# Kernel tuning notes

Hardware: AMD Instinct MI355X
Metric: run time of the kernel (lower is better)

Reference implementation:

```python
import jax, jax.numpy as jnp
import numpy as np

N_NODES = 100000
N_EDGES = 3200000


def spmm(row, col, val, x):
    # out[i] = sum_{e: row[e]==i} val[e] * x[col[e]]  -- sparse adj @ x
    return jax.ops.segment_sum(val[:, None] * x[col], row, num_segments=N_NODES)


def setup_inputs() -> dict:
    key = jax.random.key(0)
    k1, k2, k3, k4, k5, k6 = jax.random.split(key, 6)
    out_feat, hid_feat, in_feat = 32, 64, 128
    # xavier_uniform bounds
    b1 = float(np.sqrt(6.0 / (out_feat + hid_feat)))
    b2 = float(np.sqrt(6.0 / (hid_feat + in_feat)))
    return {
        "feat": jax.random.normal(k1, (N_NODES, out_feat), dtype=jnp.float32),
        "W1": jax.random.uniform(k2, (out_feat, hid_feat), minval=-b1, maxval=b1, dtype=jnp.float32),
        "W2": jax.random.uniform(k3, (hid_feat, in_feat), minval=-b2, maxval=b2, dtype=jnp.float32),
        "edge_row": jax.random.randint(k4, (N_EDGES,), 0, N_NODES, dtype=jnp.int32),
        "edge_col": jax.random.randint(k5, (N_EDGES,), 0, N_NODES, dtype=jnp.int32),
        "edge_val": jax.random.uniform(k6, (N_EDGES,), dtype=jnp.float32),
    }


def reference(feat, W1, W2, edge_row, edge_col, edge_val):
    x = feat @ W1                                  # [N, hid]
    x = spmm(edge_row, edge_col, edge_val, x)      # adj @ x
    # add_act=False: no activation
    x = x @ W2                                     # [N, in_feat]
    x = spmm(edge_row, edge_col, edge_val, x)      # adj @ x
    return x
```

## Files before the change

### kernel.cpp

```cpp
#include <hip/hip_runtime.h>

#define N_NODES 100000
#define N_EDGES 3200000
#define RPB 128
#define NB ((N_NODES + RPB - 1) / RPB)
#define SC_BLOCKS 288
#define SC_PER ((N_EDGES + SC_BLOCKS - 1) / SC_BLOCKS)
#define RS_CAP 6144

typedef unsigned short ushort_t;
typedef unsigned int uint_t;

__device__ __forceinline__ ushort_t f32_to_bf16_rne(float f) {
    uint_t b = __float_as_uint(f);
    return (ushort_t)((b + 0x7FFFu + ((b >> 16) & 1u)) >> 16);
}
__device__ __forceinline__ float bf16_lo(uint_t u) {
    return __uint_as_float(u << 16);
}
__device__ __forceinline__ float bf16_hi(uint_t u) {
    return __uint_as_float(u & 0xffff0000u);
}


__global__ void gemm_w12_kernel(const float* __restrict__ W1,
                                const float* __restrict__ W2,
                                float* __restrict__ W12) {
    int idx = blockIdx.x * blockDim.x + threadIdx.x;
    if (idx >= 32 * 128) return;
    int r = idx >> 7;
    int c = idx & 127;
    float acc = 0.f;
#pragma unroll
    for (int k = 0; k < 64; ++k) acc += W1[r * 64 + k] * W2[k * 128 + c];
    W12[idx] = acc;
}

__global__ void cvt_bf16_kernel(const float* __restrict__ in, ushort_t* __restrict__ ob) {
    int i = blockIdx.x * blockDim.x + threadIdx.x;
    if (i < N_NODES * 32) ob[i] = f32_to_bf16_rne(in[i]);
}

__global__ void gemm_out_kernel(const float* __restrict__ g2,
                                const float* __restrict__ W12,
                                float* __restrict__ out) {
    int tid = threadIdx.x;
    int jo = (tid & 31) * 4;
    int rl = tid >> 5;
    float4 w[32];
#pragma unroll
    for (int k = 0; k < 32; ++k) w[k] = *(const float4*)&W12[k * 128 + jo];
    for (int r = blockIdx.x * 8 + rl; r < N_NODES; r += gridDim.x * 8) {
        const float4* g4 = (const float4*)(g2 + (size_t)r * 32);
        float4 acc = make_float4(0.f, 0.f, 0.f, 0.f);
#pragma unroll
        for (int q = 0; q < 8; ++q) {
            float4 gv = g4[q];
            int k = q * 4;
            acc.x += gv.x * w[k].x;     acc.y += gv.x * w[k].y;
            acc.z += gv.x * w[k].z;     acc.w += gv.x * w[k].w;
            acc.x += gv.y * w[k + 1].x; acc.y += gv.y * w[k + 1].y;
            acc.z += gv.y * w[k + 1].z; acc.w += gv.y * w[k + 1].w;
            acc.x += gv.z * w[k + 2].x; acc.y += gv.z * w[k + 2].y;
            acc.z += gv.z * w[k + 2].z; acc.w += gv.z * w[k + 2].w;
            acc.x += gv.w * w[k + 3].x; acc.y += gv.w * w[k + 3].y;
            acc.z += gv.w * w[k + 3].z; acc.w += gv.w * w[k + 3].w;
        }
        *(float4*)&out[(size_t)r * 128 + jo] = acc;
    }
}


__global__ void hist_bucket_kernel(const int* __restrict__ row, int* __restrict__ cnt) {
    __shared__ int h[NB];
    for (int t = threadIdx.x; t < NB; t += blockDim.x) h[t] = 0;
    __syncthreads();
    int per = (N_EDGES + gridDim.x - 1) / gridDim.x;
    int s = blockIdx.x * per;
    int e = min(s + per, N_EDGES);
    for (int i = s + threadIdx.x; i < e; i += blockDim.x)
        atomicAdd(&h[row[i] >> 7], 1);
    __syncthreads();
    for (int t = threadIdx.x; t < NB; t += blockDim.x)
        if (h[t]) atomicAdd(&cnt[t], h[t]);
}

__global__ void scan_bucket_kernel(const int* __restrict__ cnt,
                                   int* __restrict__ offs, int* __restrict__ cur_b) {
    __shared__ int s[1024];
    int t = threadIdx.x;
    int v = (t < NB) ? cnt[t] : 0;
    s[t] = v;
    __syncthreads();
    for (int off = 1; off < 1024; off <<= 1) {
        int add = (t >= off) ? s[t - off] : 0;
        __syncthreads();
        s[t] += add;
        __syncthreads();
    }
    if (t < NB) { int x = s[t] - v; offs[t] = x; cur_b[t] = x; }
    if (t == 0) offs[NB] = N_EDGES;
}

__global__ void __launch_bounds__(1024, 1)
scatter_stage_kernel(const int* __restrict__ row, const int* __restrict__ col,
                     const float* __restrict__ val,
                     int* __restrict__ cur_b, int2* __restrict__ ebuf) {
    __shared__ int2 payload[SC_PER];
    __shared__ ushort_t bkt[SC_PER];
    __shared__ int h[NB];
    __shared__ int lbase[NB];
    __shared__ int gbase[NB];
    __shared__ int scan_s[1024];
    int t = threadIdx.x;
    int s = blockIdx.x * SC_PER;
    int e = min(s + SC_PER, N_EDGES);
    int n = e - s;
    for (int i = t; i < NB; i += 1024) h[i] = 0;
    __syncthreads();
    for (int i = t; i < n; i += 1024) atomicAdd(&h[row[s + i] >> 7], 1);
    __syncthreads();
    int v = (t < NB) ? h[t] : 0;
    scan_s[t] = v;
    __syncthreads();
    for (int off = 1; off < 1024; off <<= 1) {
        int add = (t >= off) ? scan_s[t - off] : 0;
        __syncthreads();
        scan_s[t] += add;
        __syncthreads();
    }
    if (t < NB) {
        lbase[t] = scan_s[t] - v;
        gbase[t] = v ? atomicAdd(&cur_b[t], v) : 0;
        h[t] = 0;
    }
    __syncthreads();
    for (int i = t; i < n; i += 1024) {
        int r = row[s + i];
        int b = r >> 7;
        int lp = atomicAdd(&h[b], 1);
        int slot = lbase[b] + lp;
        payload[slot] = make_int2((col[s + i] << 7) | (r & 127), __float_as_int(val[s + i]));
        bkt[slot] = (ushort_t)b;
    }
    __syncthreads();
    for (int i = t; i < n; i += 1024) {
        int b = bkt[i];
        ebuf[gbase[b] + (i - lbase[b])] = payload[i];
    }
}

__global__ void rowsort_stage_kernel(const int* __restrict__ offs, const int2* __restrict__ ebuf,
                                     int2* __restrict__ ep, int* __restrict__ rs) {
    __shared__ int h[RPB];
    __shared__ int loff[RPB];
    __shared__ int curl[RPB];
    __shared__ ushort_t perm[RS_CAP];
    int b = blockIdx.x;
    int s = offs[b], e = offs[b + 1];
    int n = e - s;
    int t = threadIdx.x;
    if (t < RPB) h[t] = 0;
    __syncthreads();
    for (int i = t; i < n; i += blockDim.x)
        atomicAdd(&h[ebuf[s + i].x & 127], 1);
    __syncthreads();
    if (t < RPB) loff[t] = h[t];
    __syncthreads();
    for (int off = 1; off < RPB; off <<= 1) {
        int add = (t < RPB && t >= off) ? loff[t - off] : 0;
        __syncthreads();
        if (t < RPB) loff[t] += add;
        __syncthreads();
    }
    if (t < RPB) {
        int excl = loff[t] - h[t];
        curl[t] = excl;
        int r = b * RPB + t;
        if (r < N_NODES) rs[r] = s + excl;
    }
    if (b == 0 && t == 0) rs[N_NODES] = N_EDGES;
    __syncthreads();
    if (n <= RS_CAP) {
        for (int i = t; i < n; i += blockDim.x) {
            int rl = ebuf[s + i].x & 127;
            int lp = atomicAdd(&curl[rl], 1);
            perm[lp] = (ushort_t)i;
        }
        __syncthreads();
        for (int i = t; i < n; i += blockDim.x) {
            int2 cv = ebuf[s + perm[i]];
            ep[s + i] = make_int2(cv.x >> 7, cv.y);
        }
    } else {
        for (int i = t; i < n; i += blockDim.x) {
            int2 cv = ebuf[s + i];
            int rl = cv.x & 127;
            int pos = s + atomicAdd(&curl[rl], 1);
            ep[pos] = make_int2(cv.x >> 7, cv.y);
        }
    }
}

template <bool OUT_BF16>
__global__ void spmm_csr_kernel(const int* __restrict__ rs,
                                const int2* __restrict__ ep,
                                const uint_t* __restrict__ xb,
                                void* __restrict__ outv) {
    int gid = blockIdx.x * blockDim.x + threadIdx.x;
    int wid = gid >> 6;
    int nwaves = (gridDim.x * blockDim.x) >> 6;
    int lane = threadIdx.x & 63;
    int j2 = lane & 15;
    int g = lane >> 4;
    for (int r = wid; r < N_NODES; r += nwaves) {
        int s = rs[r], e = rs[r + 1];
        float a0 = 0.f, a1 = 0.f, b0 = 0.f, b1 = 0.f;
        int p = s + g;
        for (; p + 28 < e; p += 32) {
            int2 c0 = ep[p];
            int2 c1 = ep[p + 4];
            int2 c2 = ep[p + 8];
            int2 c3 = ep[p + 12];
            int2 c4 = ep[p + 16];
            int2 c5 = ep[p + 20];
            int2 c6 = ep[p + 24];
            int2 c7 = ep[p + 28];
            uint_t u0 = xb[c0.x * 16 + j2];
            uint_t u1 = xb[c1.x * 16 + j2];
            uint_t u2 = xb[c2.x * 16 + j2];
            uint_t u3 = xb[c3.x * 16 + j2];
            uint_t u4 = xb[c4.x * 16 + j2];
            uint_t u5 = xb[c5.x * 16 + j2];
            uint_t u6 = xb[c6.x * 16 + j2];
            uint_t u7 = xb[c7.x * 16 + j2];
            float w0 = __int_as_float(c0.y);
            float w1 = __int_as_float(c1.y);
            float w2 = __int_as_float(c2.y);
            float w3 = __int_as_float(c3.y);
            float w4 = __int_as_float(c4.y);
            float w5 = __int_as_float(c5.y);
            float w6 = __int_as_float(c6.y);
            float w7 = __int_as_float(c7.y);
            a0 += w0 * bf16_lo(u0); a1 += w0 * bf16_hi(u0);
            b0 += w1 * bf16_lo(u1); b1 += w1 * bf16_hi(u1);
            a0 += w2 * bf16_lo(u2); a1 += w2 * bf16_hi(u2);
            b0 += w3 * bf16_lo(u3); b1 += w3 * bf16_hi(u3);
            a0 += w4 * bf16_lo(u4); a1 += w4 * bf16_hi(u4);
            b0 += w5 * bf16_lo(u5); b1 += w5 * bf16_hi(u5);
            a0 += w6 * bf16_lo(u6); a1 += w6 * bf16_hi(u6);
            b0 += w7 * bf16_lo(u7); b1 += w7 * bf16_hi(u7);
        }
        for (; p < e; p += 4) {
            int2 cv = ep[p];
            uint_t u = xb[cv.x * 16 + j2];
            float w = __int_as_float(cv.y);
            a0 += w * bf16_lo(u);
            a1 += w * bf16_hi(u);
        }
        float r0 = a0 + b0;
        float r1 = a1 + b1;
        r0 += __shfl_xor(r0, 16, 64);
        r0 += __shfl_xor(r0, 32, 64);
        r1 += __shfl_xor(r1, 16, 64);
        r1 += __shfl_xor(r1, 32, 64);
        if (g == 0) {
            if constexpr (OUT_BF16) {
                uint_t pk = (uint_t)f32_to_bf16_rne(r0) | ((uint_t)f32_to_bf16_rne(r1) << 16);
                ((uint_t*)outv)[r * 16 + j2] = pk;
            } else {
                ((float2*)outv)[r * 16 + j2] = make_float2(r0, r1);
            }
        }
    }
}

__global__ void spmm32_atomic_kernel(const int* __restrict__ row,
                                     const int* __restrict__ col,
                                     const float* __restrict__ val,
                                     const float* __restrict__ x,
                                     float* __restrict__ out) {
    int id = blockIdx.x * blockDim.x + threadIdx.x;
    int e = id >> 5;
    int j = id & 31;
    if (e >= N_EDGES) return;
    atomicAdd(&out[row[e] * 32 + j], val[e] * x[col[e] * 32 + j]);
}

__global__ void gemm_out_fallback_kernel(const float* __restrict__ g2,
                                         const float* __restrict__ W12,
                                         float* __restrict__ out) {
    int id = blockIdx.x * blockDim.x + threadIdx.x;
    int i = id >> 7;
    int j = id & 127;
    const float* g = g2 + i * 32;
    float acc = 0.f;
#pragma unroll
    for (int k = 0; k < 32; ++k) acc += g[k] * W12[k * 128 + j];
    out[id] = acc;
}

extern "C" void kernel_launch(void* const* d_in, const int* in_sizes, int n_in,
                              void* d_out, int out_size, void* d_ws, size_t ws_size,
                              hipStream_t stream) {
    const float* feat = (const float*)d_in[0];
    const float* W1   = (const float*)d_in[1];
    const float* W2   = (const float*)d_in[2];
    const int*   erow = (const int*)d_in[3];
    const int*   ecol = (const int*)d_in[4];
    const float* eval_= (const float*)d_in[5];
    float* out = (float*)d_out;

    float*    W12   = (float*)d_ws;
    ushort_t* xb    = (ushort_t*)(W12 + 4096);
    ushort_t* g1b   = xb + (size_t)N_NODES * 32;
    float*    g2    = (float*)(g1b + (size_t)N_NODES * 32);
    int2*     ep    = (int2*)(g2 + (size_t)N_NODES * 32);
    int*      cnt   = (int*)(ep + N_EDGES);
    int*      offs  = cnt + NB;
    int*      cur_b = offs + NB + 1;
    int*      rs    = cur_b + NB;
    size_t    needed = (size_t)((char*)(rs + N_NODES + 2) - (char*)d_ws);

    int2* ebuf = (int2*)d_out;

    gemm_w12_kernel<<<16, 256, 0, stream>>>(W1, W2, W12);

    if (ws_size >= needed) {
        cvt_bf16_kernel<<<(N_NODES * 32 + 255) / 256, 256, 0, stream>>>(feat, xb);

        hipMemsetAsync(cnt, 0, NB * sizeof(int), stream);
        hist_bucket_kernel<<<256, 1024, 0, stream>>>(erow, cnt);
        scan_bucket_kernel<<<1, 1024, 0, stream>>>(cnt, offs, cur_b);
        scatter_stage_kernel<<<SC_BLOCKS, 1024, 0, stream>>>(erow, ecol, eval_, cur_b, ebuf);
        rowsort_stage_kernel<<<NB, 512, 0, stream>>>(offs, ebuf, ep, rs);

        spmm_csr_kernel<true><<<2048, 256, 0, stream>>>(rs, ep, (const uint_t*)xb, g1b);
        spmm_csr_kernel<false><<<2048, 256, 0, stream>>>(rs, ep, (const uint_t*)g1b, g2);

        gemm_out_kernel<<<1024, 256, 0, stream>>>(g2, W12, out);
    } else {
        float* g1f = (float*)d_ws + 4096;
        float* g2f = g1f + (size_t)N_NODES * 32;
        hipMemsetAsync(g1f, 0, (size_t)N_NODES * 32 * 2 * sizeof(float), stream);
        spmm32_atomic_kernel<<<(N_EDGES * 32) / 256, 256, 0, stream>>>(erow, ecol, eval_, feat, g1f);
        spmm32_atomic_kernel<<<(N_EDGES * 32) / 256, 256, 0, stream>>>(erow, ecol, eval_, g1f, g2f);
        gemm_out_fallback_kernel<<<(N_NODES * 128) / 256, 256, 0, stream>>>(g2f, W12, out);
    }
}
```

Baseline: 262.4 us.

## Fuse prelude kernels, stage rowsort payload in LDS, fuse second SpMM with output GEMM

Merges the W12 product, bf16 conversion and bucket histogram into one launch. The rowsort stage now caches each bucket's edges in shared memory so the permuted copy reads LDS instead of re-reading global memory, with the capacity lowered to fit. The second SpMM now multiplies its 32-wide row result by W12 held in shared memory and writes the 128-wide output directly, which removes the g2 round trip and the separate output GEMM. The trade-off is larger LDS use per block, which may reduce occupancy, plus extra shuffle work per row.

Measured after the change: 286.6 us. +9.3%, slower.

```diff
diff --git a/kernel.cpp b/kernel.cpp
--- a/kernel.cpp
+++ b/kernel.cpp
@@ -6,7 +6,10 @@
 #define NB ((N_NODES + RPB - 1) / RPB)
 #define SC_BLOCKS 288
 #define SC_PER ((N_EDGES + SC_BLOCKS - 1) / SC_BLOCKS)
-#define RS_CAP 6144
+#define RS_CAP 4608
+#define W12_B 16
+#define CVT_B 12500
+#define HIST_B 1024
 
 typedef unsigned short ushort_t;
 typedef unsigned int uint_t;
@@ -22,67 +25,38 @@
     return __uint_as_float(u & 0xffff0000u);
 }
 
-
-__global__ void gemm_w12_kernel(const float* __restrict__ W1,
-                                const float* __restrict__ W2,
-                                float* __restrict__ W12) {
-    int idx = blockIdx.x * blockDim.x + threadIdx.x;
-    if (idx >= 32 * 128) return;
-    int r = idx >> 7;
-    int c = idx & 127;
-    float acc = 0.f;
+__global__ void prelude_kernel(const float* __restrict__ W1, const float* __restrict__ W2,
+                               float* __restrict__ W12,
+                               const float* __restrict__ feat, ushort_t* __restrict__ xb,
+                               const int* __restrict__ row, int* __restrict__ cnt) {
+    int b = blockIdx.x;
+    int t = threadIdx.x;
+    if (b < W12_B) {
+        int idx = b * 256 + t;
+        if (idx < 32 * 128) {
+            int r = idx >> 7;
+            int c = idx & 127;
+            float acc = 0.f;
 #pragma unroll
-    for (int k = 0; k < 64; ++k) acc += W1[r * 64 + k] * W2[k * 128 + c];
-    W12[idx] = acc;
-}
-
-__global__ void cvt_bf16_kernel(const float* __restrict__ in, ushort_t* __restrict__ ob) {
-    int i = blockIdx.x * blockDim.x + threadIdx.x;
-    if (i < N_NODES * 32) ob[i] = f32_to_bf16_rne(in[i]);
-}
-
-__global__ void gemm_out_kernel(const float* __restrict__ g2,
-                                const float* __restrict__ W12,
-                                float* __restrict__ out) {
-    int tid = threadIdx.x;
-    int jo = (tid & 31) * 4;
-    int rl = tid >> 5;
-    float4 w[32];
-#pragma unroll
-    for (int k = 0; k < 32; ++k) w[k] = *(const float4*)&W12[k * 128 + jo];
-    for (int r = blockIdx.x * 8 + rl; r < N_NODES; r += gridDim.x * 8) {
-        const float4* g4 = (const float4*)(g2 + (size_t)r * 32);
-        float4 acc = make_float4(0.f, 0.f, 0.f, 0.f);
-#pragma unroll
-        for (int q = 0; q < 8; ++q) {
-            float4 gv = g4[q];
-            int k = q * 4;
-            acc.x += gv.x * w[k].x;     acc.y += gv.x * w[k].y;
-            acc.z += gv.x * w[k].z;     acc.w += gv.x * w[k].w;
-            acc.x += gv.y * w[k + 1].x; acc.y += gv.y * w[k + 1].y;
-            acc.z += gv.y * w[k + 1].z; acc.w += gv.y * w[k + 1].w;
-            acc.x += gv.z * w[k + 2].x; acc.y += gv.z * w[k + 2].y;
-            acc.z += gv.z * w[k + 2].z; acc.w += gv.z * w[k + 2].w;
-            acc.x += gv.w * w[k + 3].x; acc.y += gv.w * w[k + 3].y;
-            acc.z += gv.w * w[k + 3].z; acc.w += gv.w * w[k + 3].w;
-        }
-        *(float4*)&out[(size_t)r * 128 + jo] = acc;
-    }
-}
-
-
-__global__ void hist_bucket_kernel(const int* __restrict__ row, int* __restrict__ cnt) {
-    __shared__ int h[NB];
-    for (int t = threadIdx.x; t < NB; t += blockDim.x) h[t] = 0;
-    __syncthreads();
-    int per = (N_EDGES + gridDim.x - 1) / gridDim.x;
-    int s = blockIdx.x * per;
-    int e = min(s + per, N_EDGES);
-    for (int i = s + threadIdx.x; i < e; i += blockDim.x)
-        atomicAdd(&h[row[i] >> 7], 1);
-    __syncthreads();
-    for (int t = threadIdx.x; t < NB; t += blockDim.x)
-        if (h[t]) atomicAdd(&cnt[t], h[t]);
+            for (int k = 0; k < 64; ++k) acc += W1[r * 64 + k] * W2[k * 128 + c];
+            W12[idx] = acc;
+        }
+    } else if (b < W12_B + CVT_B) {
+        int i = (b - W12_B) * 256 + t;
+        if (i < N_NODES * 32) xb[i] = f32_to_bf16_rne(feat[i]);
+    } else {
+        __shared__ int h[NB];
+        for (int i = t; i < NB; i += 256) h[i] = 0;
+        __syncthreads();
+        int hb = b - W12_B - CVT_B;
+        int per = N_EDGES / HIST_B;
+        int s = hb * per;
+        int e = min(s + per, N_EDGES);
+        for (int i = s + t; i < e; i += 256) atomicAdd(&h[row[i] >> 7], 1);
+        __syncthreads();
+        for (int i = t; i < NB; i += 256)
+            if (h[i]) atomicAdd(&cnt[i], h[i]);
+    }
 }
 
 __global__ void scan_bucket_kernel(const int* __restrict__ cnt,
@@ -152,18 +126,28 @@
 
 __global__ void rowsort_stage_kernel(const int* __restrict__ offs, const int2* __restrict__ ebuf,
                                      int2* __restrict__ ep, int* __restrict__ rs) {
+    __shared__ int2 pay[RS_CAP];
+    __shared__ ushort_t perm[RS_CAP];
     __shared__ int h[RPB];
     __shared__ int loff[RPB];
     __shared__ int curl[RPB];
-    __shared__ ushort_t perm[RS_CAP];
     int b = blockIdx.x;
     int s = offs[b], e = offs[b + 1];
     int n = e - s;
     int t = threadIdx.x;
     if (t < RPB) h[t] = 0;
     __syncthreads();
-    for (int i = t; i < n; i += blockDim.x)
-        atomicAdd(&h[ebuf[s + i].x & 127], 1);
+    bool fits = (n <= RS_CAP);
+    if (fits) {
+        for (int i = t; i < n; i += blockDim.x) {
+            int2 cv = ebuf[s + i];
+            pay[i] = cv;
+            atomicAdd(&h[cv.x & 127], 1);
+        }
+    } else {
+        for (int i = t; i < n; i += blockDim.x)
+            atomicAdd(&h[ebuf[s + i].x & 127], 1);
+    }
     __syncthreads();
     if (t < RPB) loff[t] = h[t];
     __syncthreads();
@@ -181,15 +165,14 @@
     }
     if (b == 0 && t == 0) rs[N_NODES] = N_EDGES;
     __syncthreads();
-    if (n <= RS_CAP) {
+    if (fits) {
         for (int i = t; i < n; i += blockDim.x) {
-            int rl = ebuf[s + i].x & 127;
-            int lp = atomicAdd(&curl[rl], 1);
+            int lp = atomicAdd(&curl[pay[i].x & 127], 1);
             perm[lp] = (ushort_t)i;
         }
         __syncthreads();
         for (int i = t; i < n; i += blockDim.x) {
-            int2 cv = ebuf[s + perm[i]];
+            int2 cv = pay[perm[i]];
             ep[s + i] = make_int2(cv.x >> 7, cv.y);
         }
     } else {
@@ -202,11 +185,10 @@
     }
 }
 
-template <bool OUT_BF16>
 __global__ void spmm_csr_kernel(const int* __restrict__ rs,
                                 const int2* __restrict__ ep,
                                 const uint_t* __restrict__ xb,
-                                void* __restrict__ outv) {
+                                uint_t* __restrict__ outb) {
     int gid = blockIdx.x * blockDim.x + threadIdx.x;
     int wid = gid >> 6;
     int nwaves = (gridDim.x * blockDim.x) >> 6;
@@ -265,14 +247,103 @@
         r1 += __shfl_xor(r1, 16, 64);
         r1 += __shfl_xor(r1, 32, 64);
         if (g == 0) {
-            if constexpr (OUT_BF16) {
-                uint_t pk = (uint_t)f32_to_bf16_rne(r0) | ((uint_t)f32_to_bf16_rne(r1) << 16);
-                ((uint_t*)outv)[r * 16 + j2] = pk;
-            } else {
-                ((float2*)outv)[r * 16 + j2] = make_float2(r0, r1);
-            }
-        }
-    }
+            uint_t pk = (uint_t)f32_to_bf16_rne(r0) | ((uint_t)f32_to_bf16_rne(r1) << 16);
+            outb[r * 16 + j2] = pk;
+        }
+    }
+}
+
+__global__ void spmm_fused_kernel(const int* __restrict__ rs,
+                                  const int2* __restrict__ ep,
+                                  const uint_t* __restrict__ xb,
+                                  const float* __restrict__ W12,
+                                  float* __restrict__ out) {
+    __shared__ float w12s[32 * 128];
+    for (int i = threadIdx.x; i < 32 * 128; i += blockDim.x) w12s[i] = W12[i];
+    __syncthreads();
+    int gid = blockIdx.x * blockDim.x + threadIdx.x;
+    int wid = gid >> 6;
+    int nwaves = (gridDim.x * blockDim.x) >> 6;
+    int lane = threadIdx.x & 63;
+    int j2 = lane & 15;
+    int g = lane >> 4;
+    int c0 = lane * 2;
+    for (int r = wid; r < N_NODES; r += nwaves) {
+        int s = rs[r], e = rs[r + 1];
+        float a0 = 0.f, a1 = 0.f, b0 = 0.f, b1 = 0.f;
+        int p = s + g;
+        for (; p + 28 < e; p += 32) {
+            int2 e0 = ep[p];
+            int2 e1 = ep[p + 4];
+            int2 e2 = ep[p + 8];
+            int2 e3 = ep[p + 12];
+            int2 e4 = ep[p + 16];
+            int2 e5 = ep[p + 20];
+            int2 e6 = ep[p + 24];
+            int2 e7 = ep[p + 28];
+            uint_t u0 = xb[e0.x * 16 + j2];
+            uint_t u1 = xb[e1.x * 16 + j2];
+            uint_t u2 = xb[e2.x * 16 + j2];
+            uint_t u3 = xb[e3.x * 16 + j2];
+            uint_t u4 = xb[e4.x * 16 + j2];
+            uint_t u5 = xb[e5.x * 16 + j2];
+            uint_t u6 = xb[e6.x * 16 + j2];
+            uint_t u7 = xb[e7.x * 16 + j2];
+            float w0 = __int_as_float(e0.y);
+            float w1 = __int_as_float(e1.y);
+            float w2 = __int_as_float(e2.y);
+            float w3 = __int_as_float(e3.y);
+            float w4 = __int_as_float(e4.y);
+            float w5 = __int_as_float(e5.y);
+            float w6 = __int_as_float(e6.y);
+            float w7 = __int_as_float(e7.y);
+            a0 += w0 * bf16_lo(u0); a1 += w0 * bf16_hi(u0);
+            b0 += w1 * bf16_lo(u1); b1 += w1 * bf16_hi(u1);
+            a0 += w2 * bf16_lo(u2); a1 += w2 * bf16_hi(u2);
+            b0 += w3 * bf16_lo(u3); b1 += w3 * bf16_hi(u3);
+            a0 += w4 * bf16_lo(u4); a1 += w4 * bf16_hi(u4);
+            b0 += w5 * bf16_lo(u5); b1 += w5 * bf16_hi(u5);
+            a0 += w6 * bf16_lo(u6); a1 += w6 * bf16_hi(u6);
+            b0 += w7 * bf16_lo(u7); b1 += w7 * bf16_hi(u7);
+        }
+        for (; p < e; p += 4) {
+            int2 cv = ep[p];
+            uint_t u = xb[cv.x * 16 + j2];
+            float w = __int_as_float(cv.y);
+            a0 += w * bf16_lo(u);
+            a1 += w * bf16_hi(u);
+        }
+        float r0 = a0 + b0;
+        float r1 = a1 + b1;
+        r0 += __shfl_xor(r0, 16, 64);
+        r0 += __shfl_xor(r0, 32, 64);
+        r1 += __shfl_xor(r1, 16, 64);
+        r1 += __shfl_xor(r1, 32, 64);
+        float o0 = 0.f, o1 = 0.f;
+#pragma unroll
+        for (int k = 0; k < 16; ++k) {
+            float ga = __shfl(r0, k, 64);
+            float gb = __shfl(r1, k, 64);
+            float2 wa = *(const float2*)&w12s[(2 * k) * 128 + c0];
+            float2 wb = *(const float2*)&w12s[(2 * k + 1) * 128 + c0];
+            o0 += ga * wa.x + gb * wb.x;
+            o1 += ga * wa.y + gb * wb.y;
+        }
+        *(float2*)&out[(size_t)r * 128 + c0] = make_float2(o0, o1);
+    }
+}
+
+__global__ void gemm_w12_kernel(const float* __restrict__ W1,
+                                const float* __restrict__ W2,
+                                float* __restrict__ W12) {
+    int idx = blockIdx.x * blockDim.x + threadIdx.x;
+    if (idx >= 32 * 128) return;
+    int r = idx >> 7;
+    int c = idx & 127;
+    float acc = 0.f;
+#pragma unroll
+    for (int k = 0; k < 64; ++k) acc += W1[r * 64 + k] * W2[k * 128 + c];
+    W12[idx] = acc;
 }
 
 __global__ void spmm32_atomic_kernel(const int* __restrict__ row,
@@ -324,22 +395,17 @@
 
     int2* ebuf = (int2*)d_out;
 
-    gemm_w12_kernel<<<16, 256, 0, stream>>>(W1, W2, W12);
-
     if (ws_size >= needed) {
-        cvt_bf16_kernel<<<(N_NODES * 32 + 255) / 256, 256, 0, stream>>>(feat, xb);
-
         hipMemsetAsync(cnt, 0, NB * sizeof(int), stream);
-        hist_bucket_kernel<<<256, 1024, 0, stream>>>(erow, cnt);
+        prelude_kernel<<<W12_B + CVT_B + HIST_B, 256, 0, stream>>>(W1, W2, W12, feat, xb, erow, cnt);
         scan_bucket_kernel<<<1, 1024, 0, stream>>>(cnt, offs, cur_b);
         scatter_stage_kernel<<<SC_BLOCKS, 1024, 0, stream>>>(erow, ecol, eval_, cur_b, ebuf);
         rowsort_stage_kernel<<<NB, 512, 0, stream>>>(offs, ebuf, ep, rs);
 
-        spmm_csr_kernel<true><<<2048, 256, 0, stream>>>(rs, ep, (const uint_t*)xb, g1b);
-        spmm_csr_kernel<false><<<2048, 256, 0, stream>>>(rs, ep, (const uint_t*)g1b, g2);
-
-        gemm_out_kernel<<<1024, 256, 0, stream>>>(g2, W12, out);
+        spmm_csr_kernel<<<2048, 256, 0, stream>>>(rs, ep, (const uint_t*)xb, (uint_t*)g1b);
+        spmm_fused_kernel<<<2048, 256, 0, stream>>>(rs, ep, (const uint_t*)g1b, W12, out);
     } else {
+        gemm_w12_kernel<<<16, 256, 0, stream>>>(W1, W2, W12);
         float* g1f = (float*)d_ws + 4096;
         float* g2f = g1f + (size_t)N_NODES * 32;
         hipMemsetAsync(g1f, 0, (size_t)N_NODES * 32 * 2 * sizeof(float), stream);
```

## Fuse W12 gemm, bf16 convert and histogram into one prelude; stage rowsort payload in LDS

Applied to the files above, without the earlier changes.

Three independent setup kernels (W1·W2 product, feature bf16 conversion, bucket histogram) are merged into a single launch that dispatches on block index, removing two launch gaps and letting them run concurrently. The histogram part now uses 1024 blocks of 256 threads instead of 256 of 1024. The rowsort kernel now caches each bucket's edge payload in shared memory so the permute pass reads from LDS instead of re-reading global memory. RS_CAP is lowered so the added shared buffer fits, which may send more buckets down the slow atomic-scatter fallback path.

Result: slower. 271.3 us (+3.4%).

```diff
diff --git a/kernel.cpp b/kernel.cpp
--- a/kernel.cpp
+++ b/kernel.cpp
@@ -6,7 +6,10 @@
 #define NB ((N_NODES + RPB - 1) / RPB)
 #define SC_BLOCKS 288
 #define SC_PER ((N_EDGES + SC_BLOCKS - 1) / SC_BLOCKS)
-#define RS_CAP 6144
+#define RS_CAP 4608
+#define W12_B 16
+#define CVT_B 12500
+#define HIST_B 1024
 
 typedef unsigned short ushort_t;
 typedef unsigned int uint_t;
@@ -22,67 +25,38 @@
     return __uint_as_float(u & 0xffff0000u);
 }
 
-
-__global__ void gemm_w12_kernel(const float* __restrict__ W1,
-                                const float* __restrict__ W2,
-                                float* __restrict__ W12) {
-    int idx = blockIdx.x * blockDim.x + threadIdx.x;
-    if (idx >= 32 * 128) return;
-    int r = idx >> 7;
-    int c = idx & 127;
-    float acc = 0.f;
-#pragma unroll
-    for (int k = 0; k < 64; ++k) acc += W1[r * 64 + k] * W2[k * 128 + c];
-    W12[idx] = acc;
-}
-
-__global__ void cvt_bf16_kernel(const float* __restrict__ in, ushort_t* __restrict__ ob) {
-    int i = blockIdx.x * blockDim.x + threadIdx.x;
-    if (i < N_NODES * 32) ob[i] = f32_to_bf16_rne(in[i]);
-}
-
-__global__ void gemm_out_kernel(const float* __restrict__ g2,
-                                const float* __restrict__ W12,
-                                float* __restrict__ out) {
-    int tid = threadIdx.x;
-    int jo = (tid & 31) * 4;
-    int rl = tid >> 5;
-    float4 w[32];
-#pragma unroll
-    for (int k = 0; k < 32; ++k) w[k] = *(const float4*)&W12[k * 128 + jo];
-    for (int r = blockIdx.x * 8 + rl; r < N_NODES; r += gridDim.x * 8) {
-        const float4* g4 = (const float4*)(g2 + (size_t)r * 32);
-        float4 acc = make_float4(0.f, 0.f, 0.f, 0.f);
-#pragma unroll
-        for (int q = 0; q < 8; ++q) {
-            float4 gv = g4[q];
-            int k = q * 4;
-            acc.x += gv.x * w[k].x;     acc.y += gv.x * w[k].y;
-            acc.z += gv.x * w[k].z;     acc.w += gv.x * w[k].w;
-            acc.x += gv.y * w[k + 1].x; acc.y += gv.y * w[k + 1].y;
-            acc.z += gv.y * w[k + 1].z; acc.w += gv.y * w[k + 1].w;
-            acc.x += gv.z * w[k + 2].x; acc.y += gv.z * w[k + 2].y;
-            acc.z += gv.z * w[k + 2].z; acc.w += gv.z * w[k + 2].w;
-            acc.x += gv.w * w[k + 3].x; acc.y += gv.w * w[k + 3].y;
-            acc.z += gv.w * w[k + 3].z; acc.w += gv.w * w[k + 3].w;
-        }
-        *(float4*)&out[(size_t)r * 128 + jo] = acc;
-    }
-}
-
-
-__global__ void hist_bucket_kernel(const int* __restrict__ row, int* __restrict__ cnt) {
-    __shared__ int h[NB];
-    for (int t = threadIdx.x; t < NB; t += blockDim.x) h[t] = 0;
-    __syncthreads();
-    int per = (N_EDGES + gridDim.x - 1) / gridDim.x;
-    int s = blockIdx.x * per;
-    int e = min(s + per, N_EDGES);
-    for (int i = s + threadIdx.x; i < e; i += blockDim.x)
-        atomicAdd(&h[row[i] >> 7], 1);
-    __syncthreads();
-    for (int t = threadIdx.x; t < NB; t += blockDim.x)
-        if (h[t]) atomicAdd(&cnt[t], h[t]);
+__global__ void prelude_kernel(const float* __restrict__ W1, const float* __restrict__ W2,
+                               float* __restrict__ W12,
+                               const float* __restrict__ feat, ushort_t* __restrict__ xb,
+                               const int* __restrict__ row, int* __restrict__ cnt) {
+    int b = blockIdx.x;
+    int t = threadIdx.x;
+    if (b < W12_B) {
+        int idx = b * 256 + t;
+        if (idx < 32 * 128) {
+            int r = idx >> 7;
+            int c = idx & 127;
+            float acc = 0.f;
+#pragma unroll
+            for (int k = 0; k < 64; ++k) acc += W1[r * 64 + k] * W2[k * 128 + c];
+            W12[idx] = acc;
+        }
+    } else if (b < W12_B + CVT_B) {
+        int i = (b - W12_B) * 256 + t;
+        if (i < N_NODES * 32) xb[i] = f32_to_bf16_rne(feat[i]);
+    } else {
+        __shared__ int h[NB];
+        for (int i = t; i < NB; i += 256) h[i] = 0;
+        __syncthreads();
+        int hb = b - W12_B - CVT_B;
+        int per = N_EDGES / HIST_B;
+        int s = hb * per;
+        int e = min(s + per, N_EDGES);
+        for (int i = s + t; i < e; i += 256) atomicAdd(&h[row[i] >> 7], 1);
+        __syncthreads();
+        for (int i = t; i < NB; i += 256)
+            if (h[i]) atomicAdd(&cnt[i], h[i]);
+    }
 }
 
 __global__ void scan_bucket_kernel(const int* __restrict__ cnt,
@@ -152,18 +126,28 @@
 
 __global__ void rowsort_stage_kernel(const int* __restrict__ offs, const int2* __restrict__ ebuf,
                                      int2* __restrict__ ep, int* __restrict__ rs) {
+    __shared__ int2 pay[RS_CAP];
+    __shared__ ushort_t perm[RS_CAP];
     __shared__ int h[RPB];
     __shared__ int loff[RPB];
     __shared__ int curl[RPB];
-    __shared__ ushort_t perm[RS_CAP];
     int b = blockIdx.x;
     int s = offs[b], e = offs[b + 1];
     int n = e - s;
     int t = threadIdx.x;
     if (t < RPB) h[t] = 0;
     __syncthreads();
-    for (int i = t; i < n; i += blockDim.x)
-        atomicAdd(&h[ebuf[s + i].x & 127], 1);
+    bool fits = (n <= RS_CAP);
+    if (fits) {
+        for (int i = t; i < n; i += blockDim.x) {
+            int2 cv = ebuf[s + i];
+            pay[i] = cv;
+            atomicAdd(&h[cv.x & 127], 1);
+        }
+    } else {
+        for (int i = t; i < n; i += blockDim.x)
+            atomicAdd(&h[ebuf[s + i].x & 127], 1);
+    }
     __syncthreads();
     if (t < RPB) loff[t] = h[t];
     __syncthreads();
@@ -181,15 +165,14 @@
     }
     if (b == 0 && t == 0) rs[N_NODES] = N_EDGES;
     __syncthreads();
-    if (n <= RS_CAP) {
+    if (fits) {
         for (int i = t; i < n; i += blockDim.x) {
-            int rl = ebuf[s + i].x & 127;
-            int lp = atomicAdd(&curl[rl], 1);
+            int lp = atomicAdd(&curl[pay[i].x & 127], 1);
             perm[lp] = (ushort_t)i;
         }
         __syncthreads();
         for (int i = t; i < n; i += blockDim.x) {
-            int2 cv = ebuf[s + perm[i]];
+            int2 cv = pay[perm[i]];
             ep[s + i] = make_int2(cv.x >> 7, cv.y);
         }
     } else {
@@ -275,6 +258,48 @@
     }
 }
 
+__global__ void gemm_out_kernel(const float* __restrict__ g2,
+                                const float* __restrict__ W12,
+                                float* __restrict__ out) {
+    int tid = threadIdx.x;
+    int jo = (tid & 31) * 4;
+    int rl = tid >> 5;
+    float4 w[32];
+#pragma unroll
+    for (int k = 0; k < 32; ++k) w[k] = *(const float4*)&W12[k * 128 + jo];
+    for (int r = blockIdx.x * 8 + rl; r < N_NODES; r += gridDim.x * 8) {
+        const float4* g4 = (const float4*)(g2 + (size_t)r * 32);
+        float4 acc = make_float4(0.f, 0.f, 0.f, 0.f);
+#pragma unroll
+        for (int q = 0; q < 8; ++q) {
+            float4 gv = g4[q];
+            int k = q * 4;
+            acc.x += gv.x * w[k].x;     acc.y += gv.x * w[k].y;
+            acc.z += gv.x * w[k].z;     acc.w += gv.x * w[k].w;
+            acc.x += gv.y * w[k + 1].x; acc.y += gv.y * w[k + 1].y;
+            acc.z += gv.y * w[k + 1].z; acc.w += gv.y * w[k + 1].w;
+            acc.x += gv.z * w[k + 2].x; acc.y += gv.z * w[k + 2].y;
+            acc.z += gv.z * w[k + 2].z; acc.w += gv.z * w[k + 2].w;
+            acc.x += gv.w * w[k + 3].x; acc.y += gv.w * w[k + 3].y;
+            acc.z += gv.w * w[k + 3].z; acc.w += gv.w * w[k + 3].w;
+        }
+        *(float4*)&out[(size_t)r * 128 + jo] = acc;
+    }
+}
+
+__global__ void gemm_w12_kernel(const float* __restrict__ W1,
+                                const float* __restrict__ W2,
+                                float* __restrict__ W12) {
+    int idx = blockIdx.x * blockDim.x + threadIdx.x;
+    if (idx >= 32 * 128) return;
+    int r = idx >> 7;
+    int c = idx & 127;
+    float acc = 0.f;
+#pragma unroll
+    for (int k = 0; k < 64; ++k) acc += W1[r * 64 + k] * W2[k * 128 + c];
+    W12[idx] = acc;
+}
+
 __global__ void spmm32_atomic_kernel(const int* __restrict__ row,
                                      const int* __restrict__ col,
                                      const float* __restrict__ val,
@@ -324,13 +349,9 @@
 
     int2* ebuf = (int2*)d_out;
 
-    gemm_w12_kernel<<<16, 256, 0, stream>>>(W1, W2, W12);
-
     if (ws_size >= needed) {
-        cvt_bf16_kernel<<<(N_NODES * 32 + 255) / 256, 256, 0, stream>>>(feat, xb);
-
         hipMemsetAsync(cnt, 0, NB * sizeof(int), stream);
-        hist_bucket_kernel<<<256, 1024, 0, stream>>>(erow, cnt);
+        prelude_kernel<<<W12_B + CVT_B + HIST_B, 256, 0, stream>>>(W1, W2, W12, feat, xb, erow, cnt);
         scan_bucket_kernel<<<1, 1024, 0, stream>>>(cnt, offs, cur_b);
         scatter_stage_kernel<<<SC_BLOCKS, 1024, 0, stream>>>(erow, ecol, eval_, cur_b, ebuf);
         rowsort_stage_kernel<<<NB, 512, 0, stream>>>(offs, ebuf, ep, rs);
@@ -340,6 +361,7 @@
 
         gemm_out_kernel<<<1024, 256, 0, stream>>>(g2, W12, out);
     } else {
+        gemm_w12_kernel<<<16, 256, 0, stream>>>(W1, W2, W12);
         float* g1f = (float*)d_ws + 4096;
         float* g2f = g1f + (size_t)N_NODES * 32;
         hipMemsetAsync(g1f, 0, (size_t)N_NODES * 32 * 2 * sizeof(float), stream);
```
